# Performance work log

Hardware: AMD Instinct MI355X
Metric: run time of the kernel (lower is better)

Reference implementation:

```python
import jax, jax.numpy as jnp
import numpy as np

B, N_IN, N_HID, N_OUT, N_CLUST = 4096, 32, 128, 30000, 10000
BN_EPS = 1e-3  # scvi FCLayers uses BatchNorm1d(eps=0.001)


def setup_inputs() -> dict:
    key = jax.random.key(0)
    ks = jax.random.split(key, 4)
    z = jax.random.normal(ks[0], (B, N_IN), dtype=jnp.float32)
    W1 = jax.random.normal(ks[1], (N_HID, N_IN), dtype=jnp.float32) * 0.1
    b1 = jnp.zeros((N_HID,), dtype=jnp.float32)
    gamma = jnp.ones((N_HID,), dtype=jnp.float32)
    beta = jnp.zeros((N_HID,), dtype=jnp.float32)
    W2 = jax.random.normal(ks[2], (N_OUT, N_HID), dtype=jnp.float32) * 0.05
    b2 = jnp.zeros((N_OUT,), dtype=jnp.float32)
    # 3 introns per cluster, sorted cluster ids; first intron of each cluster
    intron_clusters = (jnp.arange(N_OUT, dtype=jnp.int32) // 3).astype(jnp.int32)
    first_indices = (jnp.arange(N_CLUST, dtype=jnp.int32) * 3).astype(jnp.int32)
    return {"z": z, "W1": W1, "b1": b1, "gamma": gamma, "beta": beta,
            "W2": W2, "b2": b2, "intron_clusters": intron_clusters,
            "first_indices": first_indices}


def reference(z, W1, b1, gamma, beta, W2, b2, intron_clusters, first_indices):
    # FCLayers (1 layer, dropout=0): Linear -> BatchNorm1d (batch stats) -> ReLU
    h = z @ W1.T + b1                                   # [B, n_hidden]
    mu = jnp.mean(h, axis=0)
    var = jnp.var(h, axis=0)
    h = gamma * (h - mu) * jax.lax.rsqrt(var + BN_EPS) + beta
    h = jax.nn.relu(h)
    # second_part Linear
    potentials = h @ W2.T + b2                          # [B, n_output]
    # pin first intron of each cluster to 0 (scatter-zero mask)
    potentials = potentials.at[:, first_indices].set(0.0)
    p_u = jnp.exp(potentials)                           # [B, n_output]
    # sparse cluster_summation @ p_u.T  ==  segment sum over introns per cluster
    cluster_sums = jax.ops.segment_sum(p_u.T, intron_clusters,
                                       num_segments=N_CLUST).T  # [B, n_clusters]
    # gather each intron's cluster sum and normalize (segment softmax)
    norm_factor = cluster_sums[:, intron_clusters]      # [B, n_output]
    return p_u / norm_factor
```

## Files before the change

### kernel.cpp

```cpp
#include <hip/hip_runtime.h>
#include <hip/hip_bf16.h>


typedef float  floatx4 __attribute__((ext_vector_type(4)));
typedef __bf16 bf16x8  __attribute__((ext_vector_type(8)));
typedef __bf16 bf16x4  __attribute__((ext_vector_type(4)));

struct F3 { float x, y, z; };

#define GLOBAL_AS __attribute__((address_space(1)))
#define LDS_AS    __attribute__((address_space(3)))

__device__ __forceinline__ void async16(void* lds, const void* g) {
    __builtin_amdgcn_global_load_lds((const GLOBAL_AS void*)g, (LDS_AS void*)lds, 16, 0, 0);
}

__global__ __launch_bounds__(256) void k_hidden_cvt(const float* __restrict__ z,
                                                    const float* __restrict__ W1,
                                                    const float* __restrict__ b1,
                                                    float* __restrict__ h,
                                                    float* __restrict__ stats,
                                                    const float* __restrict__ w2,
                                                    __bf16* __restrict__ w2b) {
    const int bid = blockIdx.x;
    const int tid = threadIdx.x;
    if (bid >= 256) {
        const int i  = (bid - 256) * 256 + tid;
        const int rp = i >> 4;
        const int c  = i & 15;
        const int nb = rp >> 5, n = rp & 31;
        const int src = nb * 48 + 3 * (n & 15) + 1 + (n >> 4);
        const float* s = w2 + (size_t)src * 128 + c * 8;
        floatx4 v0 = *(const floatx4*)s;
        floatx4 v1 = *(const floatx4*)(s + 4);
        bf16x8 o;
        o[0] = (__bf16)v0[0]; o[1] = (__bf16)v0[1]; o[2] = (__bf16)v0[2]; o[3] = (__bf16)v0[3];
        o[4] = (__bf16)v1[0]; o[5] = (__bf16)v1[1]; o[6] = (__bf16)v1[2]; o[7] = (__bf16)v1[3];
        *(bf16x8*)(w2b + (size_t)rp * 128 + c * 8) = o;
        return;
    }
    __shared__ float sW1[128 * 33];
    __shared__ float sz[16 * 32];
    __shared__ float red[256];
    const int rb = bid * 16;
    for (int i = tid; i < 128 * 32; i += 256) sW1[(i >> 5) * 33 + (i & 31)] = W1[i];
    for (int i = tid; i < 16 * 32; i += 256) sz[i] = z[rb * 32 + i];
    __syncthreads();
    const int col = tid & 127, rh = tid >> 7;
    const float bias = b1[col];
    float lsum = 0.f, lsq = 0.f;
    for (int r = rh; r < 16; r += 2) {
        float acc = bias;
#pragma unroll
        for (int k = 0; k < 32; ++k) acc += sz[r * 32 + k] * sW1[col * 33 + k];
        h[(rb + r) * 128 + col] = acc;
        lsum += acc; lsq += acc * acc;
    }
    red[tid] = lsum; __syncthreads();
    if (rh == 0) atomicAdd(&stats[col], red[col] + red[col + 128]);
    __syncthreads();
    red[tid] = lsq; __syncthreads();
    if (rh == 0) atomicAdd(&stats[128 + col], red[col] + red[col + 128]);
}

__global__ __launch_bounds__(256) void k_norm(const float* __restrict__ h,
                                              const float* __restrict__ stats,
                                              const float* __restrict__ gamma,
                                              const float* __restrict__ beta,
                                              __bf16* __restrict__ hb) {
    const int idx = blockIdx.x * 256 + threadIdx.x;
    const int c0  = (idx * 4) & 127;
    floatx4 v = *(const floatx4*)(h + (size_t)idx * 4);
    bf16x4 o;
#pragma unroll
    for (int j = 0; j < 4; ++j) {
        const int col = c0 + j;
        const float mu  = stats[col] * (1.0f / 4096.0f);
        const float var = stats[128 + col] * (1.0f / 4096.0f) - mu * mu;
        const float sc  = gamma[col] * rsqrtf(var + 1e-3f);
        const float sh  = beta[col] - mu * sc;
        o[j] = (__bf16)fmaxf(v[j] * sc + sh, 0.0f);
    }
    *(bf16x4*)(hb + (size_t)idx * 4) = o;
}

__global__ __launch_bounds__(256, 3) void k_main(const __bf16* __restrict__ hb,
                                                 const __bf16* __restrict__ w2b,
                                                 const float* __restrict__ b2,
                                                 float* __restrict__ out) {
    __shared__ __align__(16) char smem[49152];
    char* smemA = smem;
    char* smemB = smem + 32768;
    const int tid    = threadIdx.x;
    const int rowblk = blockIdx.x;
    const int y      = blockIdx.y;
    const int row0   = rowblk * 128;
    const int ulim   = (y == 312) ? 1 : 2;

    {
        const char* g = (const char*)(hb + (size_t)row0 * 128);
#pragma unroll
        for (int it = 0; it < 8; ++it) {
            int L = it * 256 + tid;
            int row = L >> 4, c = L & 15;
            int gc = (c & 8) | ((c ^ row) & 7);
            async16(smemA + L * 16, g + (row * 16 + gc) * 16);
        }
    }
    {
        const char* g = (const char*)(w2b + (size_t)y * 64 * 128);
#pragma unroll
        for (int it = 0; it < 4; ++it) {
            int L = it * 256 + tid;
            int n = L >> 4, c = L & 15;
            int gc = (c & 8) | ((c ^ n) & 7);
            int nn = (n < 32 * ulim) ? n : (n - 32);
            async16(smemB + L * 16, g + (nn * 16 + gc) * 16);
        }
    }

    const int lane = tid & 63, w = tid >> 6;
    const int quad = lane >> 4, lr = lane & 15;
    const int cb0 = y * 96 + 3 * lr;
    float bb1[2], bb2[2];
    bb1[0] = b2[cb0 + 1]; bb2[0] = b2[cb0 + 2];
    if (ulim > 1) { bb1[1] = b2[cb0 + 49]; bb2[1] = b2[cb0 + 50]; }
    else          { bb1[1] = 0.f;          bb2[1] = 0.f; }
    __syncthreads();

    const floatx4 z4 = {0.f, 0.f, 0.f, 0.f};
    floatx4 acc[2][2][2];
#pragma unroll
    for (int s = 0; s < 2; ++s)
#pragma unroll
        for (int u = 0; u < 2; ++u)
#pragma unroll
            for (int t = 0; t < 2; ++t) acc[s][u][t] = z4;

#pragma unroll
    for (int ks = 0; ks < 4; ++ks) {
        const int cg = ks * 4 + quad;
        bf16x8 a[2], b[2][2];
#pragma unroll
        for (int s = 0; s < 2; ++s) {
            int r  = w * 32 + s * 16 + lr;
            int ch = (cg & 8) | ((cg ^ r) & 7);
            a[s] = *(const bf16x8*)(smemA + r * 256 + ch * 16);
        }
#pragma unroll
        for (int u = 0; u < 2; ++u)
#pragma unroll
            for (int t = 0; t < 2; ++t) {
                int n  = u * 32 + t * 16 + lr;
                int ch = (cg & 8) | ((cg ^ n) & 7);
                b[u][t] = *(const bf16x8*)(smemB + n * 256 + ch * 16);
            }
#pragma unroll
        for (int s = 0; s < 2; ++s)
#pragma unroll
            for (int u = 0; u < 2; ++u)
#pragma unroll
                for (int t = 0; t < 2; ++t)
                    acc[s][u][t] = __builtin_amdgcn_mfma_f32_16x16x32_bf16(a[s], b[u][t], acc[s][u][t], 0, 0, 0);
    }

#pragma unroll
    for (int s = 0; s < 2; ++s) {
#pragma unroll
        for (int u = 0; u < 2; ++u) {
            if (u < ulim) {
#pragma unroll
                for (int r = 0; r < 4; ++r) {
                    int m = row0 + w * 32 + s * 16 + quad * 4 + r;
                    float v1  = __expf(acc[s][u][0][r] + bb1[u]);
                    float v2  = __expf(acc[s][u][1][r] + bb2[u]);
                    float inv = __builtin_amdgcn_rcpf(1.0f + v1 + v2);
                    F3 o; o.x = inv; o.y = v1 * inv; o.z = v2 * inv;
                    *(F3*)(out + (size_t)m * 30000 + cb0 + u * 48) = o;
                }
            }
        }
    }
}

extern "C" void kernel_launch(void* const* d_in, const int* in_sizes, int n_in,
                              void* d_out, int out_size, void* d_ws, size_t ws_size,
                              hipStream_t stream) {
    const float* z     = (const float*)d_in[0];
    const float* W1    = (const float*)d_in[1];
    const float* b1    = (const float*)d_in[2];
    const float* gamma = (const float*)d_in[3];
    const float* beta  = (const float*)d_in[4];
    const float* W2    = (const float*)d_in[5];
    const float* b2    = (const float*)d_in[6];
    float* out = (float*)d_out;

    char* ws = (char*)d_ws;
    float*  h     = (float*)ws;
    __bf16* hb    = (__bf16*)(ws + (2u << 20));
    __bf16* w2b   = (__bf16*)(ws + (3u << 20));
    float*  stats = (float*)(ws + (11u << 20));

    hipMemsetAsync(stats, 0, 256 * sizeof(float), stream);
    k_hidden_cvt<<<1506, 256, 0, stream>>>(z, W1, b1, h, stats, W2, w2b);
    k_norm<<<512, 256, 0, stream>>>(h, stats, gamma, beta, hb);
    dim3 grid(32, 313);
    k_main<<<grid, 256, 0, stream>>>(hb, w2b, b2, out);
}
```

Measured before the change: 542.5 us.

## Load MFMA fragments directly from global memory, drop LDS staging

The main GEMM kernel no longer stages the hidden and W2 tiles in shared memory with async global-to-LDS copies and a block barrier. Each wave now loads its bf16 A and B fragments straight into registers from global memory in MFMA layout, and the epilogue loops are reordered so each output row pointer is computed once. The aim is to remove the 48KB LDS footprint and the __syncthreads stall, which could allow more resident blocks and let stores overlap better. In exchange, the B tile is fetched separately by all four waves through the caches. For the last column block the u=1 loads read past the valid W2 rows, though those values are never used.

New measurement: 599.2 us. 10.4% more time.

```diff
diff --git a/kernel.cpp b/kernel.cpp
--- a/kernel.cpp
+++ b/kernel.cpp
@@ -7,13 +7,6 @@
 typedef __bf16 bf16x4  __attribute__((ext_vector_type(4)));
 
 struct F3 { float x, y, z; };
-
-#define GLOBAL_AS __attribute__((address_space(1)))
-#define LDS_AS    __attribute__((address_space(3)))
-
-__device__ __forceinline__ void async16(void* lds, const void* g) {
-    __builtin_amdgcn_global_load_lds((const GLOBAL_AS void*)g, (LDS_AS void*)lds, 16, 0, 0);
-}
 
 __global__ __launch_bounds__(256) void k_hidden_cvt(const float* __restrict__ z,
                                                     const float* __restrict__ W1,
@@ -88,45 +81,30 @@
                                                  const __bf16* __restrict__ w2b,
                                                  const float* __restrict__ b2,
                                                  float* __restrict__ out) {
-    __shared__ __align__(16) char smem[49152];
-    char* smemA = smem;
-    char* smemB = smem + 32768;
     const int tid    = threadIdx.x;
     const int rowblk = blockIdx.x;
     const int y      = blockIdx.y;
     const int row0   = rowblk * 128;
     const int ulim   = (y == 312) ? 1 : 2;
 
-    {
-        const char* g = (const char*)(hb + (size_t)row0 * 128);
-#pragma unroll
-        for (int it = 0; it < 8; ++it) {
-            int L = it * 256 + tid;
-            int row = L >> 4, c = L & 15;
-            int gc = (c & 8) | ((c ^ row) & 7);
-            async16(smemA + L * 16, g + (row * 16 + gc) * 16);
-        }
-    }
-    {
-        const char* g = (const char*)(w2b + (size_t)y * 64 * 128);
-#pragma unroll
-        for (int it = 0; it < 4; ++it) {
-            int L = it * 256 + tid;
-            int n = L >> 4, c = L & 15;
-            int gc = (c & 8) | ((c ^ n) & 7);
-            int nn = (n < 32 * ulim) ? n : (n - 32);
-            async16(smemB + L * 16, g + (nn * 16 + gc) * 16);
-        }
-    }
-
     const int lane = tid & 63, w = tid >> 6;
     const int quad = lane >> 4, lr = lane & 15;
+
     const int cb0 = y * 96 + 3 * lr;
     float bb1[2], bb2[2];
     bb1[0] = b2[cb0 + 1]; bb2[0] = b2[cb0 + 2];
     if (ulim > 1) { bb1[1] = b2[cb0 + 49]; bb2[1] = b2[cb0 + 50]; }
     else          { bb1[1] = 0.f;          bb2[1] = 0.f; }
-    __syncthreads();
+
+    const char* Ab = (const char*)hb + (size_t)(row0 + w * 32 + lr) * 256 + quad * 16;
+    bf16x8 a[4][2];
+#pragma unroll
+    for (int ks = 0; ks < 4; ++ks)
+#pragma unroll
+        for (int s = 0; s < 2; ++s)
+            a[ks][s] = *(const bf16x8*)(Ab + s * (16 * 256) + ks * 64);
+
+    const char* Bb = (const char*)w2b + (size_t)(y * 64 + lr) * 256 + quad * 16;
 
     const floatx4 z4 = {0.f, 0.f, 0.f, 0.f};
     floatx4 acc[2][2][2];
@@ -138,45 +116,36 @@
             for (int t = 0; t < 2; ++t) acc[s][u][t] = z4;
 
 #pragma unroll
-    for (int ks = 0; ks < 4; ++ks) {
-        const int cg = ks * 4 + quad;
-        bf16x8 a[2], b[2][2];
+    for (int u = 0; u < 2; ++u) {
+        bf16x8 bv[4][2];
 #pragma unroll
-        for (int s = 0; s < 2; ++s) {
-            int r  = w * 32 + s * 16 + lr;
-            int ch = (cg & 8) | ((cg ^ r) & 7);
-            a[s] = *(const bf16x8*)(smemA + r * 256 + ch * 16);
-        }
+        for (int ks = 0; ks < 4; ++ks)
 #pragma unroll
-        for (int u = 0; u < 2; ++u)
+            for (int t = 0; t < 2; ++t)
+                bv[ks][t] = *(const bf16x8*)(Bb + (u * 32 + t * 16) * 256 + ks * 64);
 #pragma unroll
-            for (int t = 0; t < 2; ++t) {
-                int n  = u * 32 + t * 16 + lr;
-                int ch = (cg & 8) | ((cg ^ n) & 7);
-                b[u][t] = *(const bf16x8*)(smemB + n * 256 + ch * 16);
-            }
+        for (int ks = 0; ks < 4; ++ks)
 #pragma unroll
-        for (int s = 0; s < 2; ++s)
-#pragma unroll
-            for (int u = 0; u < 2; ++u)
+            for (int s = 0; s < 2; ++s)
 #pragma unroll
                 for (int t = 0; t < 2; ++t)
-                    acc[s][u][t] = __builtin_amdgcn_mfma_f32_16x16x32_bf16(a[s], b[u][t], acc[s][u][t], 0, 0, 0);
+                    acc[s][u][t] = __builtin_amdgcn_mfma_f32_16x16x32_bf16(a[ks][s], bv[ks][t], acc[s][u][t], 0, 0, 0);
     }
 
 #pragma unroll
     for (int s = 0; s < 2; ++s) {
 #pragma unroll
-        for (int u = 0; u < 2; ++u) {
-            if (u < ulim) {
+        for (int r = 0; r < 4; ++r) {
+            int m = row0 + w * 32 + s * 16 + quad * 4 + r;
+            float* prow = out + (size_t)m * 30000 + cb0;
 #pragma unroll
-                for (int r = 0; r < 4; ++r) {
-                    int m = row0 + w * 32 + s * 16 + quad * 4 + r;
+            for (int u = 0; u < 2; ++u) {
+                if (u < ulim) {
                     float v1  = __expf(acc[s][u][0][r] + bb1[u]);
                     float v2  = __expf(acc[s][u][1][r] + bb2[u]);
                     float inv = __builtin_amdgcn_rcpf(1.0f + v1 + v2);
                     F3 o; o.x = inv; o.y = v1 * inv; o.z = v2 * inv;
-                    *(F3*)(out + (size_t)m * 30000 + cb0 + u * 48) = o;
+                    *(F3*)(prow + u * 48) = o;
                 }
             }
         }
```
